# Kernel optimization log

Measured on AMD Instinct MI355X. Metric: run time of the kernel, lower is better.

## Reference

```python
import jax, jax.numpy as jnp
import numpy as np

MODEL_DIM = 1024
NUM_HEADS = 16
K_DIM = MODEL_DIM // NUM_HEADS


def setup_inputs() -> dict:
    key = jax.random.key(0)
    kx, kw1, kw2 = jax.random.split(key, 3)
    B, L, D = 4, 2048, MODEL_DIM
    x = jax.random.normal(kx, (B, L, D), dtype=jnp.float32)
    # nn.Linear(D, 3D, bias=False): y = x @ W^T; store transposed form [D, 3D]
    scale1 = 1.0 / np.sqrt(D)
    Wqkv = jax.random.uniform(kw1, (D, 3 * D), dtype=jnp.float32, minval=-scale1, maxval=scale1)
    Wout = jax.random.uniform(kw2, (D, D), dtype=jnp.float32, minval=-scale1, maxval=scale1)
    return {"x": x, "Wqkv": Wqkv, "Wout": Wout}


def reference(x, Wqkv, Wout):
    B, L, D = x.shape
    H, Kd = NUM_HEADS, K_DIM
    qkv = x @ Wqkv  # [B, L, 3D]
    q, k, v = jnp.split(qkv, 3, axis=-1)

    def heads(t):  # [B, L, D] -> [B, H, L, Kd]
        return t.reshape(B, L, H, Kd).transpose(0, 2, 1, 3)

    qh, kh, vh = heads(q), heads(k), heads(v)
    scores = jnp.einsum('bhqd,bhkd->bhqk', qh, kh) / jnp.sqrt(jnp.float32(Kd))
    causal = jnp.triu(jnp.ones((L, L), dtype=bool), k=1)  # True above diagonal
    scores = jnp.where(causal, -jnp.inf, scores)
    probs = jax.nn.softmax(scores, axis=-1)
    attended = jnp.einsum('bhqk,bhkd->bhqd', probs, vh)
    concatted = attended.transpose(0, 2, 1, 3).reshape(B, L, D)
    # dropout is identity in eval mode
    return concatted @ Wout
```

## Files before the change

kernel.cpp:

```cpp
#include <hip/hip_runtime.h>

typedef unsigned short u16;
typedef unsigned int   u32;
typedef __bf16   bf16x8 __attribute__((ext_vector_type(8)));
typedef float    f32x4  __attribute__((ext_vector_type(4)));
typedef u16      u16x4  __attribute__((ext_vector_type(4)));
typedef u16      u16x8  __attribute__((ext_vector_type(8)));
typedef u32      u32x2  __attribute__((ext_vector_type(2)));
typedef u32      u32x4  __attribute__((ext_vector_type(4)));

#if __has_builtin(__builtin_amdgcn_exp2f)
#define EXP2(x) __builtin_amdgcn_exp2f(x)
#else
#define EXP2(x) exp2f(x)
#endif

__device__ __forceinline__ u16 f2bf(float f) {
    unsigned u = __float_as_uint(f);
    u += 0x7FFFu + ((u >> 16) & 1u);
    return (u16)(u >> 16);
}

__device__ __forceinline__ u32 pack_bf16(float a, float b) {
#if __has_builtin(__builtin_amdgcn_cvt_pk_bf16_f32)
    typedef __bf16 bf16x2 __attribute__((ext_vector_type(2)));
    bf16x2 r = __builtin_amdgcn_cvt_pk_bf16_f32(a, b);
    return __builtin_bit_cast(u32, r);
#else
    return (u32)f2bf(a) | ((u32)f2bf(b) << 16);
#endif
}

__device__ __forceinline__ void async_copy16(const u16* g, u16* l) {
    __builtin_amdgcn_global_load_lds(
        (const __attribute__((address_space(1))) unsigned*)g,
        (__attribute__((address_space(3))) unsigned*)l, 16, 0, 0);
}

__device__ __forceinline__ bf16x8 lds_frag(const u16* p) {
    return *(const bf16x8*)p;
}

__device__ __forceinline__ void permlane32_swap(u32& a, u32& b) {
    asm("v_permlane32_swap_b32 %0, %1" : "+v"(a), "+v"(b));
}
__device__ __forceinline__ void permlane16_swap(u32& a, u32& b) {
    asm("v_permlane16_swap_b32 %0, %1" : "+v"(a), "+v"(b));
}

__global__ __launch_bounds__(256) void prep(const float* __restrict__ x,
                                            const float* __restrict__ Wqkv,
                                            const float* __restrict__ Wout,
                                            u16* __restrict__ xb,
                                            u16* __restrict__ wqkv_t,
                                            u16* __restrict__ wout_t) {
    __shared__ u16 t[64 * 72];
    const int bid = blockIdx.x;
    const int tid = threadIdx.x;

    if (bid >= 1024) {
        size_t i = ((size_t)(bid - 1024) * 256 + tid) * 8;
        float4 v0 = *(const float4*)(x + i);
        float4 v1 = *(const float4*)(x + i + 4);
        u16x8 o = { f2bf(v0.x), f2bf(v0.y), f2bf(v0.z), f2bf(v0.w),
                    f2bf(v1.x), f2bf(v1.y), f2bf(v1.z), f2bf(v1.w) };
        *(u16x8*)(xb + i) = o;
        return;
    }

    const float* W;  u16* Wt;  int Kd, Nd, n0, k0;
    if (bid < 768) { W = Wqkv; Wt = wqkv_t; Kd = 1024; Nd = 3072;
                     n0 = (bid % 48) * 64; k0 = (bid / 48) * 64; }
    else           { W = Wout; Wt = wout_t; Kd = 1024; Nd = 1024;
                     n0 = ((bid - 768) % 16) * 64; k0 = ((bid - 768) / 16) * 64; }
#pragma unroll
    for (int i = 0; i < 4; ++i) {
        int lin = i * 256 + tid;
        int kr = lin >> 4, nc = (lin & 15) << 2;
        float4 v = *(const float4*)(W + (size_t)(k0 + kr) * Nd + n0 + nc);
        u16x4 o = { f2bf(v.x), f2bf(v.y), f2bf(v.z), f2bf(v.w) };
        *(u16x4*)&t[kr * 72 + nc] = o;
    }
    __syncthreads();
#pragma unroll
    for (int i = 0; i < 2; ++i) {
        int lin = i * 256 + tid;
        int nr = lin >> 3, kc = (lin & 7) << 3;
        u16x8 o;
#pragma unroll
        for (int jj = 0; jj < 8; ++jj) o[jj] = t[(kc + jj) * 72 + nr];
        *(u16x8*)(Wt + (size_t)(n0 + nr) * Kd + k0 + kc) = o;
    }
}

__global__ __launch_bounds__(256) void gemm_qkv(const u16* __restrict__ A,
                                                const u16* __restrict__ Bt,
                                                u16* __restrict__ outb,
                                                int K, int N) {
    __shared__ u16 As[2][128 * 32];
    __shared__ u16 Bs[2][128 * 32];
    const int tid = threadIdx.x;
    const int lane = tid & 63;
    const int wv = tid >> 6;
    const int wr = (wv >> 1) * 64;
    const int wc = (wv & 1) * 64;
    const int qd = lane >> 4;
    const int c  = lane & 15;

    const int flat = blockIdx.x;
    const int r_ = flat & 7;
    const int q_ = flat >> 3;
    const int m0 = ((r_ >> 1) * 16 + q_ / 12) * 128;
    const int n0 = ((r_ & 1) * 12 + q_ % 12) * 128;

    const int srow = tid >> 2;
    const int sg = ((tid & 3) ^ ((srow >> 1) & 3)) << 3;

    const u16* Ag0 = A  + (size_t)(m0 +      srow) * K + sg;
    const u16* Ag1 = A  + (size_t)(m0 + 64 + srow) * K + sg;
    const u16* Bg0 = Bt + (size_t)(n0 +      srow) * K + sg;
    const u16* Bg1 = Bt + (size_t)(n0 + 64 + srow) * K + sg;

    const u32 fsw = (qd ^ ((c >> 1) & 3)) << 3;
    const u32 a_off = (wr + c) * 32 + fsw;
    const u32 b_off = (wc + c) * 32 + fsw;

    f32x4 acc[4][4] = {};

    async_copy16(Ag0, &As[0][tid * 8]);
    async_copy16(Ag1, &As[0][2048 + tid * 8]);
    async_copy16(Bg0, &Bs[0][tid * 8]);
    async_copy16(Bg1, &Bs[0][2048 + tid * 8]);

    int p = 0;
    for (int k0 = 0; k0 < K; k0 += 32) {
        __syncthreads();
        if (k0 + 32 < K) {
            const int np = p ^ 1;
            async_copy16(Ag0 + k0 + 32, &As[np][tid * 8]);
            async_copy16(Ag1 + k0 + 32, &As[np][2048 + tid * 8]);
            async_copy16(Bg0 + k0 + 32, &Bs[np][tid * 8]);
            async_copy16(Bg1 + k0 + 32, &Bs[np][2048 + tid * 8]);
        }
        bf16x8 af[4], bfr[4];
#pragma unroll
        for (int i = 0; i < 4; ++i) af[i]  = lds_frag(&As[p][a_off + i * 512]);
#pragma unroll
        for (int j = 0; j < 4; ++j) bfr[j] = lds_frag(&Bs[p][b_off + j * 512]);
#pragma unroll
        for (int i = 0; i < 4; ++i)
#pragma unroll
            for (int j = 0; j < 4; ++j)
                acc[i][j] = __builtin_amdgcn_mfma_f32_16x16x32_bf16(af[i], bfr[j], acc[i][j], 0, 0, 0);
        p ^= 1;
    }

#pragma unroll
    for (int i = 0; i < 4; ++i)
#pragma unroll
        for (int j = 0; j < 4; ++j) {
            int n = n0 + wc + j * 16 + c;
            int which = n >> 10, h = (n >> 6) & 15, kd = n & 63;
            int m_base = m0 + wr + i * 16 + qd * 4;
            int b = m_base >> 11, l0 = m_base & 2047;
            int bh = b * 16 + h;
            if (which == 2) {
                u32x2 o2;
                o2[0] = pack_bf16(acc[i][j][0], acc[i][j][1]);
                o2[1] = pack_bf16(acc[i][j][2], acc[i][j][3]);
                *(u32x2*)(outb + (size_t)(128 + bh) * 131072 + (size_t)kd * 2048 + l0) = o2;
            } else if (which == 0) {
#pragma unroll
                for (int r = 0; r < 4; ++r)
                    outb[(size_t)bh * 131072 + (size_t)(l0 + r) * 64 + kd] =
                        f2bf(acc[i][j][r] * 0.1803368801f);
            } else {
#pragma unroll
                for (int r = 0; r < 4; ++r)
                    outb[(size_t)(64 + bh) * 131072 + (size_t)(l0 + r) * 64 + kd] =
                        f2bf(acc[i][j][r]);
            }
        }
}

__global__ __launch_bounds__(256) void gemm_out(const u16* __restrict__ A,
                                                const u16* __restrict__ Bt,
                                                float* __restrict__ outf,
                                                int K, int N) {
    __shared__ u16 As[2][128 * 64];
    __shared__ u16 Bs[2][128 * 64];
    const int tid = threadIdx.x;
    const int lane = tid & 63;
    const int wv = tid >> 6;
    const int wr = (wv >> 1) * 64;
    const int wc = (wv & 1) * 64;
    const int qd = lane >> 4;
    const int c  = lane & 15;

    const int flat = blockIdx.x;
    const int r_ = flat & 7;
    const int q_ = flat >> 3;
    const int m0 = (r_ * 8 + (q_ >> 3)) * 128;
    const int n0 = (q_ & 7) * 128;

    auto stage = [&](int t, int slot) {
        const int kb = t * 64;
#pragma unroll
        for (int it = 0; it < 4; ++it) {
            int lin = it * 256 + tid;
            int row = lin >> 3;
            int sch = ((lin & 7) ^ (row & 7)) << 3;
            async_copy16(A  + (size_t)(m0 + row) * K + kb + sch,
                         &As[slot][lin * 8]);
            async_copy16(Bt + (size_t)(n0 + row) * K + kb + sch,
                         &Bs[slot][lin * 8]);
        }
    };

    const u32 a_base = (wr + c) * 64;
    const u32 b_base = (wc + c) * 64;
    const u32 ch0 = (u32)((qd ^ (c & 7)) << 3);
    const u32 ch1 = (u32)(((4 + qd) ^ (c & 7)) << 3);

    f32x4 acc[4][4] = {};

    stage(0, 0);

    const int NT = K >> 6;
    int p = 0;
#pragma unroll 1
    for (int kt = 0; kt < NT; ++kt) {
        __syncthreads();
        if (kt + 1 < NT) stage(kt + 1, p ^ 1);

        bf16x8 af[4], bfr[4];
#pragma unroll
        for (int i = 0; i < 4; ++i) af[i]  = lds_frag(&As[p][a_base + i * 1024 + ch0]);
#pragma unroll
        for (int j = 0; j < 4; ++j) bfr[j] = lds_frag(&Bs[p][b_base + j * 1024 + ch0]);
#pragma unroll
        for (int i = 0; i < 4; ++i)
#pragma unroll
            for (int j = 0; j < 4; ++j)
                acc[i][j] = __builtin_amdgcn_mfma_f32_16x16x32_bf16(af[i], bfr[j], acc[i][j], 0, 0, 0);
#pragma unroll
        for (int i = 0; i < 4; ++i) af[i]  = lds_frag(&As[p][a_base + i * 1024 + ch1]);
#pragma unroll
        for (int j = 0; j < 4; ++j) bfr[j] = lds_frag(&Bs[p][b_base + j * 1024 + ch1]);
#pragma unroll
        for (int i = 0; i < 4; ++i)
#pragma unroll
            for (int j = 0; j < 4; ++j)
                acc[i][j] = __builtin_amdgcn_mfma_f32_16x16x32_bf16(af[i], bfr[j], acc[i][j], 0, 0, 0);
        p ^= 1;
    }

#pragma unroll
    for (int i = 0; i < 4; ++i)
#pragma unroll
        for (int j = 0; j < 4; ++j) {
            int n = n0 + wc + j * 16 + c;
            int m_base = m0 + wr + i * 16 + qd * 4;
#pragma unroll
            for (int r = 0; r < 4; ++r)
                outf[(size_t)(m_base + r) * N + n] = acc[i][j][r];
        }
}

#define ATTN_S(KSB, QA, QB)                                                   \
    do {                                                                      \
        _Pragma("unroll") for (int f = 0; f < 8; ++f) {                       \
            sa[f] = f32x4{-8.f, -8.f, -8.f, -8.f};                            \
            sb[f] = f32x4{-8.f, -8.f, -8.f, -8.f};                            \
        }                                                                     \
        __builtin_amdgcn_s_setprio(1);                                        \
        _Pragma("unroll") for (int ks = 0; ks < 2; ++ks) {                    \
            const u16* kp = (KSB) + kf_off[ks];                               \
            _Pragma("unroll") for (int f = 0; f < 8; ++f) {                   \
                bf16x8 kf = lds_frag(kp + f * 1024);                          \
                sa[f] = __builtin_amdgcn_mfma_f32_16x16x32_bf16(              \
                    kf, QA[ks], sa[f], 0, 0, 0);                              \
                sb[f] = __builtin_amdgcn_mfma_f32_16x16x32_bf16(              \
                    kf, QB[ks], sb[f], 0, 0, 0);                              \
            }                                                                 \
        }                                                                     \
        __builtin_amdgcn_s_setprio(0);                                        \
    } while (0)

#define ATTN_FIN(VTB, KT, QT, QAROW, QBROW, RVA, RVB, ACCA, ACCB)             \
    do {                                                                      \
        if ((KT) == (QT)) {                                                   \
            _Pragma("unroll") for (int f = 0; f < 8; ++f)                     \
                _Pragma("unroll") for (int r = 0; r < 4; ++r) {               \
                    int key = (KT) * 128 + f * 16 + qd * 4 + r;               \
                    if (key > (QAROW)) sa[f][r] = -3e38f;                     \
                    if (key > (QBROW)) sb[f][r] = -3e38f;                     \
                }                                                             \
        }                                                                     \
        _Pragma("unroll") for (int f = 0; f < 8; ++f) {                       \
            _Pragma("unroll") for (int r = 0; r < 4; ++r) {                   \
                sa[f][r] = EXP2(sa[f][r]);                                    \
                sb[f][r] = EXP2(sb[f][r]);                                    \
            }                                                                 \
            RVA += sa[f];                                                     \
            RVB += sb[f];                                                     \
        }                                                                     \
        _Pragma("unroll") for (int kc = 0; kc < 4; ++kc) {                    \
            u32 a0 = pack_bf16(sa[2 * kc][0], sa[2 * kc][1]);                 \
            u32 a1 = pack_bf16(sa[2 * kc + 1][0], sa[2 * kc + 1][1]);         \
            u32 b0 = pack_bf16(sa[2 * kc][2], sa[2 * kc][3]);                 \
            u32 b1 = pack_bf16(sa[2 * kc + 1][2], sa[2 * kc + 1][3]);         \
            permlane32_swap(a0, a1); permlane16_swap(a0, a1);                 \
            permlane32_swap(b0, b1); permlane16_swap(b0, b1);                 \
            u32x4 wpa = {a0, b0, a1, b1};                                     \
            bf16x8 pa = __builtin_bit_cast(bf16x8, wpa);                      \
            u32 c0 = pack_bf16(sb[2 * kc][0], sb[2 * kc][1]);                 \
            u32 c1 = pack_bf16(sb[2 * kc + 1][0], sb[2 * kc + 1][1]);         \
            u32 d0 = pack_bf16(sb[2 * kc][2], sb[2 * kc][3]);                 \
            u32 d1 = pack_bf16(sb[2 * kc + 1][2], sb[2 * kc + 1][3]);         \
            permlane32_swap(c0, c1); permlane16_swap(c0, c1);                 \
            permlane32_swap(d0, d1); permlane16_swap(d0, d1);                 \
            u32x4 wpb = {c0, d0, c1, d1};                                     \
            bf16x8 pb = __builtin_bit_cast(bf16x8, wpb);                      \
            const u16* vp = (VTB) + vf_off[kc];                               \
            __builtin_amdgcn_s_setprio(1);                                    \
            _Pragma("unroll") for (int jo = 0; jo < 4; ++jo) {                \
                bf16x8 vf = lds_frag(vp + jo * 2048);                         \
                ACCA[jo] = __builtin_amdgcn_mfma_f32_16x16x32_bf16(           \
                    vf, pa, ACCA[jo], 0, 0, 0);                               \
                ACCB[jo] = __builtin_amdgcn_mfma_f32_16x16x32_bf16(           \
                    vf, pb, ACCB[jo], 0, 0, 0);                               \
            }                                                                 \
            __builtin_amdgcn_s_setprio(0);                                    \
        }                                                                     \
    } while (0)

__global__ __launch_bounds__(256) void attn_kernel(const u16* __restrict__ qkv,
                                                   u16* __restrict__ att) {
    __shared__ u16 Ks[128 * 64];
    __shared__ u16 Vt[64 * 128];

    const int tid = threadIdx.x;
    const int lane = tid & 63;
    const int w = tid >> 6;
    const int qd = lane >> 4;
    const int c = lane & 15;

    const int idx = blockIdx.x;
    const int g = idx >> 8;
    const int s = (idx >> 6) & 3;
    const int bh = idx & 63;
    const int qt = (g & 1) ? (15 - 2 * s - (g >> 1)) : (2 * s + (g >> 1));
    const int b = bh >> 4, h = bh & 15;

    const u16* Qg = qkv + (size_t)bh * 131072;
    const u16* Kg = qkv + (size_t)(64 + bh) * 131072;
    const u16* Vg = qkv + (size_t)(128 + bh) * 131072;

    u32 kf_off[2];
#pragma unroll
    for (int ks = 0; ks < 2; ++ks)
        kf_off[ks] = c * 64 + (((ks * 4 + qd) ^ (c & 7)) << 3);
    u32 vf_off[4];
#pragma unroll
    for (int kc = 0; kc < 4; ++kc)
        vf_off[kc] = c * 128 + (((kc * 4 + qd) ^ c) << 3);

    auto issue_copy = [&](int t) {
#pragma unroll
        for (int it = 0; it < 4; ++it) {
            int lin = it * 256 + tid;
            int krw = lin >> 3, kch = lin & 7;
            int vrw = lin >> 4, vch = lin & 15;
            async_copy16(Kg + (size_t)t * 8192 + krw * 64 + ((kch ^ (krw & 7)) << 3),
                         Ks + lin * 8);
            async_copy16(Vg + (size_t)t * 128 + (size_t)vrw * 2048 + ((vch ^ (vrw & 15)) << 3),
                         Vt + lin * 8);
        }
    };

    const int NT = qt + 1;

    const int qa_row = qt * 128 + w * 32 + c;
    const int qb_row = qa_row + 16;

    bf16x8 qa[2], qb[2];
#pragma unroll
    for (int ks = 0; ks < 2; ++ks) {
        qa[ks] = *(const bf16x8*)(Qg + (size_t)qa_row * 64 + ks * 32 + qd * 8);
        qb[ks] = *(const bf16x8*)(Qg + (size_t)qb_row * 64 + ks * 32 + qd * 8);
    }

    f32x4 acca[4] = {}, accb[4] = {};
    f32x4 rva = {}, rvb = {};
    f32x4 sa[8], sb[8];

#pragma unroll 1
    for (int kt = 0; kt < NT; ++kt) {
        issue_copy(kt);
        __syncthreads();
        ATTN_S(Ks, qa, qb);
        ATTN_FIN(Vt, kt, qt, qa_row, qb_row, rva, rvb, acca, accb);
        if (kt + 1 < NT) __syncthreads();
    }

    float ra = rva[0] + rva[1] + rva[2] + rva[3];
    float rb = rvb[0] + rvb[1] + rvb[2] + rvb[3];
    ra += __shfl_xor(ra, 16, 64);
    ra += __shfl_xor(ra, 32, 64);
    rb += __shfl_xor(rb, 16, 64);
    rb += __shfl_xor(rb, 32, 64);
    float ia = __builtin_amdgcn_rcpf(ra), ib = __builtin_amdgcn_rcpf(rb);
    u16* ar = att + ((size_t)b * 2048 + qa_row) * 1024 + h * 64;
    u16* br = att + ((size_t)b * 2048 + qb_row) * 1024 + h * 64;
#pragma unroll
    for (int jo = 0; jo < 4; ++jo) {
        u32x2 oa, ob;
        oa[0] = pack_bf16(acca[jo][0] * ia, acca[jo][1] * ia);
        oa[1] = pack_bf16(acca[jo][2] * ia, acca[jo][3] * ia);
        ob[0] = pack_bf16(accb[jo][0] * ib, accb[jo][1] * ib);
        ob[1] = pack_bf16(accb[jo][2] * ib, accb[jo][3] * ib);
        *(u32x2*)(ar + jo * 16 + qd * 4) = oa;
        *(u32x2*)(br + jo * 16 + qd * 4) = ob;
    }
}

extern "C" void kernel_launch(void* const* d_in, const int* in_sizes, int n_in,
                              void* d_out, int out_size, void* d_ws, size_t ws_size,
                              hipStream_t stream) {
    const float* x    = (const float*)d_in[0];
    const float* Wqkv = (const float*)d_in[1];
    const float* Wout = (const float*)d_in[2];
    float* out = (float*)d_out;

    char* ws = (char*)d_ws;
    u16* x_bf   = (u16*)(ws);
    u16* wqkv_t = (u16*)(ws + 16777216);
    u16* wout_t = (u16*)(ws + 23068672);
    u16* qkv_h  = (u16*)(ws + 25165824);
    u16* att    = (u16*)(ws + 75497472);

    prep<<<dim3(5120), dim3(256), 0, stream>>>(x, Wqkv, Wout, x_bf, wqkv_t, wout_t);
    gemm_qkv<<<dim3(1536), dim3(256), 0, stream>>>(x_bf, wqkv_t, qkv_h, 1024, 3072);
    attn_kernel<<<dim3(1024), dim3(256), 0, stream>>>(qkv_h, att);
    gemm_out<<<dim3(512), dim3(256), 0, stream>>>(att, wout_t, out, 1024, 1024);
}
```

Before: 249.3 us.

## Double-buffer 64-key K/V tiles in attention to overlap loads with compute

```diff
diff --git a/kernel.cpp b/kernel.cpp
--- a/kernel.cpp
+++ b/kernel.cpp
@@ -269,14 +269,14 @@
 
 #define ATTN_S(KSB, QA, QB)                                                   \
     do {                                                                      \
-        _Pragma("unroll") for (int f = 0; f < 8; ++f) {                       \
+        _Pragma("unroll") for (int f = 0; f < 4; ++f) {                       \
             sa[f] = f32x4{-8.f, -8.f, -8.f, -8.f};                            \
             sb[f] = f32x4{-8.f, -8.f, -8.f, -8.f};                            \
         }                                                                     \
         __builtin_amdgcn_s_setprio(1);                                        \
         _Pragma("unroll") for (int ks = 0; ks < 2; ++ks) {                    \
             const u16* kp = (KSB) + kf_off[ks];                               \
-            _Pragma("unroll") for (int f = 0; f < 8; ++f) {                   \
+            _Pragma("unroll") for (int f = 0; f < 4; ++f) {                   \
                 bf16x8 kf = lds_frag(kp + f * 1024);                          \
                 sa[f] = __builtin_amdgcn_mfma_f32_16x16x32_bf16(              \
                     kf, QA[ks], sa[f], 0, 0, 0);                              \
@@ -287,25 +287,25 @@
         __builtin_amdgcn_s_setprio(0);                                        \
     } while (0)
 
-#define ATTN_FIN(VTB, KT, QT, QAROW, QBROW, RVA, RVB, ACCA, ACCB)             \
+#define ATTN_FIN(VTB, KT)                                                     \
     do {                                                                      \
-        if ((KT) == (QT)) {                                                   \
-            _Pragma("unroll") for (int f = 0; f < 8; ++f)                     \
+        if ((KT) >= qt2) {                                                    \
+            _Pragma("unroll") for (int f = 0; f < 4; ++f)                     \
                 _Pragma("unroll") for (int r = 0; r < 4; ++r) {               \
-                    int key = (KT) * 128 + f * 16 + qd * 4 + r;               \
-                    if (key > (QAROW)) sa[f][r] = -3e38f;                     \
-                    if (key > (QBROW)) sb[f][r] = -3e38f;                     \
+                    int key = (KT) * 64 + f * 16 + qd * 4 + r;                \
+                    if (key > qa_row) sa[f][r] = -3e38f;                      \
+                    if (key > qb_row) sb[f][r] = -3e38f;                      \
                 }                                                             \
         }                                                                     \
-        _Pragma("unroll") for (int f = 0; f < 8; ++f) {                       \
+        _Pragma("unroll") for (int f = 0; f < 4; ++f) {                       \
             _Pragma("unroll") for (int r = 0; r < 4; ++r) {                   \
                 sa[f][r] = EXP2(sa[f][r]);                                    \
                 sb[f][r] = EXP2(sb[f][r]);                                    \
             }                                                                 \
-            RVA += sa[f];                                                     \
-            RVB += sb[f];                                                     \
+            rva += sa[f];                                                     \
+            rvb += sb[f];                                                     \
         }                                                                     \
-        _Pragma("unroll") for (int kc = 0; kc < 4; ++kc) {                    \
+        _Pragma("unroll") for (int kc = 0; kc < 2; ++kc) {                    \
             u32 a0 = pack_bf16(sa[2 * kc][0], sa[2 * kc][1]);                 \
             u32 a1 = pack_bf16(sa[2 * kc + 1][0], sa[2 * kc + 1][1]);         \
             u32 b0 = pack_bf16(sa[2 * kc][2], sa[2 * kc][3]);                 \
@@ -325,20 +325,20 @@
             const u16* vp = (VTB) + vf_off[kc];                               \
             __builtin_amdgcn_s_setprio(1);                                    \
             _Pragma("unroll") for (int jo = 0; jo < 4; ++jo) {                \
-                bf16x8 vf = lds_frag(vp + jo * 2048);                         \
-                ACCA[jo] = __builtin_amdgcn_mfma_f32_16x16x32_bf16(           \
-                    vf, pa, ACCA[jo], 0, 0, 0);                               \
-                ACCB[jo] = __builtin_amdgcn_mfma_f32_16x16x32_bf16(           \
-                    vf, pb, ACCB[jo], 0, 0, 0);                               \
+                bf16x8 vf = lds_frag(vp + jo * 1024);                         \
+                acca[jo] = __builtin_amdgcn_mfma_f32_16x16x32_bf16(           \
+                    vf, pa, acca[jo], 0, 0, 0);                               \
+                accb[jo] = __builtin_amdgcn_mfma_f32_16x16x32_bf16(           \
+                    vf, pb, accb[jo], 0, 0, 0);                               \
             }                                                                 \
             __builtin_amdgcn_s_setprio(0);                                    \
         }                                                                     \
     } while (0)
 
-__global__ __launch_bounds__(256) void attn_kernel(const u16* __restrict__ qkv,
-                                                   u16* __restrict__ att) {
-    __shared__ u16 Ks[128 * 64];
-    __shared__ u16 Vt[64 * 128];
+__global__ __launch_bounds__(256, 4) void attn_kernel(const u16* __restrict__ qkv,
+                                                      u16* __restrict__ att) {
+    __shared__ u16 Ks[2][64 * 64];
+    __shared__ u16 Vt[2][64 * 64];
 
     const int tid = threadIdx.x;
     const int lane = tid & 63;
@@ -351,6 +351,7 @@
     const int s = (idx >> 6) & 3;
     const int bh = idx & 63;
     const int qt = (g & 1) ? (15 - 2 * s - (g >> 1)) : (2 * s + (g >> 1));
+    const int qt2 = 2 * qt;
     const int b = bh >> 4, h = bh & 15;
 
     const u16* Qg = qkv + (size_t)bh * 131072;
@@ -361,25 +362,24 @@
 #pragma unroll
     for (int ks = 0; ks < 2; ++ks)
         kf_off[ks] = c * 64 + (((ks * 4 + qd) ^ (c & 7)) << 3);
-    u32 vf_off[4];
-#pragma unroll
-    for (int kc = 0; kc < 4; ++kc)
-        vf_off[kc] = c * 128 + (((kc * 4 + qd) ^ c) << 3);
-
-    auto issue_copy = [&](int t) {
-#pragma unroll
-        for (int it = 0; it < 4; ++it) {
+    u32 vf_off[2];
+#pragma unroll
+    for (int kc = 0; kc < 2; ++kc)
+        vf_off[kc] = c * 64 + (((kc * 4 + qd) ^ (c & 7)) << 3);
+
+    auto issue_copy = [&](int t, u16* kd_, u16* vd_) {
+#pragma unroll
+        for (int it = 0; it < 2; ++it) {
             int lin = it * 256 + tid;
-            int krw = lin >> 3, kch = lin & 7;
-            int vrw = lin >> 4, vch = lin & 15;
-            async_copy16(Kg + (size_t)t * 8192 + krw * 64 + ((kch ^ (krw & 7)) << 3),
-                         Ks + lin * 8);
-            async_copy16(Vg + (size_t)t * 128 + (size_t)vrw * 2048 + ((vch ^ (vrw & 15)) << 3),
-                         Vt + lin * 8);
+            int rw = lin >> 3, chn = lin & 7;
+            async_copy16(Kg + (size_t)(t * 64 + rw) * 64 + ((chn ^ (rw & 7)) << 3),
+                         kd_ + lin * 8);
+            async_copy16(Vg + (size_t)rw * 2048 + t * 64 + ((chn ^ (rw & 7)) << 3),
+                         vd_ + lin * 8);
         }
     };
 
-    const int NT = qt + 1;
+    const int NT = qt2 + 2;
 
     const int qa_row = qt * 128 + w * 32 + c;
     const int qb_row = qa_row + 16;
@@ -393,15 +393,21 @@
 
     f32x4 acca[4] = {}, accb[4] = {};
     f32x4 rva = {}, rvb = {};
-    f32x4 sa[8], sb[8];
+    f32x4 sa[4], sb[4];
+
+    issue_copy(0, Ks[0], Vt[0]);
+    __syncthreads();
+    issue_copy(1, Ks[1], Vt[1]);
 
 #pragma unroll 1
     for (int kt = 0; kt < NT; ++kt) {
-        issue_copy(kt);
-        __syncthreads();
-        ATTN_S(Ks, qa, qb);
-        ATTN_FIN(Vt, kt, qt, qa_row, qb_row, rva, rvb, acca, accb);
-        if (kt + 1 < NT) __syncthreads();
+        const int p = kt & 1;
+        ATTN_S(Ks[p], qa, qb);
+        ATTN_FIN(Vt[p], kt);
+        if (kt + 1 < NT) {
+            __syncthreads();
+            if (kt + 2 < NT) issue_copy(kt + 2, Ks[p], Vt[p]);
+        }
     }
 
     float ra = rva[0] + rva[1] + rva[2] + rva[3];
```

After: 238.6 us. 1.04x faster.
